# Optimization experiments

Measured on AMD Instinct MI355X. Metric: run time of the kernel, lower is better.

The kernel has to match this reference:

```python
import jax, jax.numpy as jnp
import numpy as np

D_MODEL = 512
HIDDEN = 2 * D_MODEL
B, L = 8, 2048
R_MIN, R_MAX = 0.8, 0.99
LN_EPS = 1e-5


def setup_inputs() -> dict:
    key = jax.random.key(0)
    ks = jax.random.split(key, 12)
    x = jax.random.normal(ks[0], (B, L, D_MODEL), jnp.float32)
    mask = jnp.ones((B, L), jnp.float32)
    # LRU eigenvalue init, exactly as the torch __init__
    u1 = jax.random.uniform(ks[1], (HIDDEN,), jnp.float32)
    u2 = jax.random.uniform(ks[2], (HIDDEN,), jnp.float32)
    nu_log = jnp.log(-0.5 * jnp.log(u1 * (R_MAX ** 2 - R_MIN ** 2) + R_MIN ** 2))
    theta_log = jnp.log(u2 * 2.0 * np.pi)
    diag_lambda = jnp.exp(jax.lax.complex(-jnp.exp(nu_log), jnp.exp(theta_log)))
    gamma_log = jnp.log(jnp.sqrt(1.0 - jnp.abs(diag_lambda) ** 2))
    params_log = jnp.stack([nu_log, theta_log, gamma_log])  # (3, HIDDEN)
    s_in = 1.0 / np.sqrt(D_MODEL)
    s_out = 1.0 / np.sqrt(HIDDEN)
    # complex Linear weights (real+imag parts; trained weights are fully complex)
    W_in_re = jax.random.uniform(ks[3], (HIDDEN, D_MODEL), jnp.float32, -s_in, s_in)
    W_in_im = jax.random.uniform(ks[4], (HIDDEN, D_MODEL), jnp.float32, -s_in, s_in)
    b_in_re = jax.random.uniform(ks[5], (HIDDEN,), jnp.float32, -s_in, s_in)
    b_in_im = jax.random.uniform(ks[6], (HIDDEN,), jnp.float32, -s_in, s_in)
    W_out_re = jax.random.uniform(ks[7], (D_MODEL, HIDDEN), jnp.float32, -s_out, s_out)
    W_out_im = jax.random.uniform(ks[8], (D_MODEL, HIDDEN), jnp.float32, -s_out, s_out)
    b_out_re = jax.random.uniform(ks[9], (D_MODEL,), jnp.float32, -s_out, s_out)
    b_out_im = jax.random.uniform(ks[10], (D_MODEL,), jnp.float32, -s_out, s_out)
    ln_w = jnp.ones((D_MODEL,), jnp.float32)
    ln_b = jnp.zeros((D_MODEL,), jnp.float32)
    return dict(x=x, mask=mask, params_log=params_log,
                W_in_re=W_in_re, W_in_im=W_in_im, b_in_re=b_in_re, b_in_im=b_in_im,
                W_out_re=W_out_re, W_out_im=W_out_im, b_out_re=b_out_re, b_out_im=b_out_im,
                ln_w=ln_w, ln_b=ln_b)


def _lru_parallel_scan(h, lamb, mask, Bn, Ln, Dn):
    # log-depth doubling trick over complex diagonal recurrence (faithful port)
    log2_L = int(np.ceil(np.log2(Ln)))
    for i in range(1, log2_L + 1):
        l = 2 ** i
        h = h.reshape(Bn * Ln // l, l, Dn)
        m = mask.reshape(Bn * Ln // l, l)
        h1, h2 = h[:, : l // 2], h[:, l // 2 :]
        if i > 1:
            lamb = jnp.concatenate([lamb, lamb * lamb[-1]], axis=0)  # powers lam^1..lam^(l/2)
        h2 = h2 + lamb * h1[:, -1:] * m[:, l // 2 - 1 : l // 2, None]
        h = jnp.concatenate([h1, h2], axis=1)
    return h.reshape(Bn, Ln, Dn)


def reference(x, mask, params_log, W_in_re, W_in_im, b_in_re, b_in_im,
              W_out_re, W_out_im, b_out_re, b_out_im, ln_w, ln_b):
    nu, theta, gamma = jnp.exp(params_log)  # each (HIDDEN,)
    lamb = jnp.exp(jax.lax.complex(-nu, theta))[None, :]  # (1, HIDDEN)
    W_in = jax.lax.complex(W_in_re, W_in_im)
    b_in = jax.lax.complex(b_in_re, b_in_im)
    W_out = jax.lax.complex(W_out_re, W_out_im)
    b_out = jax.lax.complex(b_out_re, b_out_im)
    xc = x.astype(jnp.complex64)
    h = (jnp.einsum('bld,hd->blh', xc, W_in) + b_in) * gamma  # (B, L, HIDDEN) complex64
    Bn, Ln, Dn = h.shape
    h = _lru_parallel_scan(h, lamb, mask, Bn, Ln, Dn)
    y = (jnp.einsum('blh,dh->bld', h, W_out) + b_out).real + x  # dropout = identity (eval)
    mean = jnp.mean(y, axis=-1, keepdims=True)
    var = jnp.var(y, axis=-1, keepdims=True)
    return (y - mean) / jnp.sqrt(var + LN_EPS) * ln_w + ln_b
```

## Files before the change

kernel.cpp:

```cpp
#include <hip/hip_runtime.h>
#include <hip/hip_bf16.h>
#include <cstdint>
#include <cstddef>


typedef unsigned short u16;
typedef __attribute__((ext_vector_type(8))) short bf16x8;
typedef __attribute__((ext_vector_type(4))) float f32x4;

#define B_    8
#define L_    2048
#define D_    512
#define H_    1024
#define M_    (B_ * L_)
#define SEG_  64
#define T_    (L_ / SEG_)

__device__ __forceinline__ float b2f(u16 u) {
  union { unsigned int i; float f; } v; v.i = ((unsigned int)u) << 16; return v.f;
}
__device__ __forceinline__ u16 f2b(float f) {
  union { float f; unsigned int i; } v; v.f = f;
  unsigned int x = v.i;
  return (u16)((x + 0x7fffu + ((x >> 16) & 1u)) >> 16);
}

__device__ __forceinline__ void gl2lds16(const void* g, void* l) {
  __builtin_amdgcn_global_load_lds(
      (const __attribute__((address_space(1))) void*)g,
      (__attribute__((address_space(3))) void*)l, 16, 0, 0);
}

__device__ __forceinline__ int ksw8(int row, int c) {
  return (c ^ (row & 7)) & 7;
}

__global__ __launch_bounds__(256) void prep_all(
    const float* __restrict__ x, u16* __restrict__ xb,
    const float* __restrict__ wire, const float* __restrict__ wiim,
    const float* __restrict__ wore, const float* __restrict__ woim,
    const float* __restrict__ bire, const float* __restrict__ biim,
    const float* __restrict__ params,
    u16* __restrict__ winb, u16* __restrict__ wcat, float* __restrict__ bb)
{
  int i = blockIdx.x * 256 + threadIdx.x;
#pragma unroll
  for (int j = 0; j < 4; ++j) {
    int gi = i + j * 524288;
    float4 v = ((const float4*)x)[gi];
    ushort4 o;
    o.x = f2b(v.x); o.y = f2b(v.y); o.z = f2b(v.z); o.w = f2b(v.w);
    ((ushort4*)xb)[gi] = o;
  }
  {
    int cp = i >> 9, k = i & 511;
    float g = expf(params[2 * H_ + cp]);
    winb[(size_t)(2 * cp) * 512 + k]     = f2b(wire[i] * g);
    winb[(size_t)(2 * cp + 1) * 512 + k] = f2b(wiim[i] * g);
  }
  {
    int d = i >> 10, c = i & 1023;
    wcat[(size_t)d * 2048 + 2 * c]     = f2b(wore[i]);
    wcat[(size_t)d * 2048 + 2 * c + 1] = f2b(-woim[i]);
  }
  if (i < 1024) {
    float gb = expf(params[2 * H_ + i]);
    bb[2 * i]     = bire[i] * gb;
    bb[2 * i + 1] = biim[i] * gb;
  }
}

__global__ __launch_bounds__(256, 4) void gemm_scan(
    const u16* __restrict__ A, const u16* __restrict__ Bp,
    const float* __restrict__ mask, const float* __restrict__ params,
    u16* __restrict__ h, const float* __restrict__ bb,
    float2* __restrict__ segfin, float* __restrict__ prodm)
{
  __shared__ __align__(16) u16 sAB[16384];
  __shared__ float mf[128];
  const int K = 512;

  const int tid  = threadIdx.x;
  const int lane = tid & 63;
  const int wave = tid >> 6;
  const int wm = wave >> 1, wn = wave & 1;
  const int m0 = blockIdx.x * 128;
  const int n0 = blockIdx.y * 128;
  const int b  = m0 >> 11;
  const int local0 = m0 & (L_ - 1);

  f32x4 acc[4][4];
#pragma unroll
  for (int i = 0; i < 4; ++i)
#pragma unroll
    for (int j = 0; j < 4; ++j) { f32x4 z = {0.f, 0.f, 0.f, 0.f}; acc[i][j] = z; }

  const int q = lane >> 4;
  const int r = lane & 15;

  for (int k0 = 0; k0 < K; k0 += 64) {
#pragma unroll
    for (int it = 0; it < 4; ++it) {
      int ci  = it * 256 + tid;
      int row = ci >> 3;
      int kc  = ksw8(row, ci & 7);
      gl2lds16(A  + (size_t)(m0 + row) * K + k0 + kc * 8, &sAB[ci * 8]);
      gl2lds16(Bp + (size_t)(n0 + row) * K + k0 + kc * 8, &sAB[8192 + ci * 8]);
    }
    __syncthreads();
#pragma unroll
    for (int kk = 0; kk < 2; ++kk) {
      const int cs = kk * 4 + q;
      bf16x8 af[4], bfv[4];
#pragma unroll
      for (int mt = 0; mt < 4; ++mt) {
        int arow = wm * 64 + mt * 16 + r;
        af[mt] = *(const bf16x8*)&sAB[(arow * 8 + ksw8(arow, cs)) * 8];
      }
#pragma unroll
      for (int nt = 0; nt < 4; ++nt) {
        int brow = wn * 64 + nt * 16 + r;
        bfv[nt] = *(const bf16x8*)&sAB[8192 + (brow * 8 + ksw8(brow, cs)) * 8];
      }
#pragma unroll
      for (int mt = 0; mt < 4; ++mt)
#pragma unroll
        for (int nt = 0; nt < 4; ++nt)
          acc[mt][nt] = __builtin_amdgcn_mfma_f32_16x16x32_bf16(
              bfv[nt], af[mt], acc[mt][nt], 0, 0, 0);
    }
    __syncthreads();
  }

  u16* sH = sAB;
  if (tid < 128)
    mf[tid] = (local0 + tid == 0) ? 0.f
                                  : mask[b * L_ + local0 + tid - 1];
#pragma unroll
  for (int mt = 0; mt < 4; ++mt) {
    const int trow = wm * 64 + mt * 16 + r;
    const int sw = (trow & 7) << 4;
#pragma unroll
    for (int nt = 0; nt < 4; ++nt) {
      const int nc = wn * 64 + nt * 16 + q * 4;
      const float4 b4 = *(const float4*)&bb[n0 + nc];
      ushort4 o;
      o.x = f2b(acc[mt][nt][0] + b4.x);
      o.y = f2b(acc[mt][nt][1] + b4.y);
      o.z = f2b(acc[mt][nt][2] + b4.z);
      o.w = f2b(acc[mt][nt][3] + b4.w);
      *(ushort4*)&sH[trow * 128 + (nc ^ sw)] = o;
    }
  }
  __syncthreads();

#pragma unroll
  for (int it = 0; it < 8; ++it) {
    int flat = it * 256 + tid;
    int row  = flat >> 4;
    int c16  = (flat & 15) * 8;
    bf16x8 v = *(const bf16x8*)&sH[row * 128 + (c16 ^ ((row & 7) << 4))];
    *(bf16x8*)&h[(size_t)(m0 + row) * 2048 + n0 + c16] = v;
  }

  {
    const int sIdx = wave;
    const int cpG  = (n0 >> 1) + lane;
    float nu = expf(params[cpG]);
    float th = expf(params[H_ + cpG]);
    float mg = expf(-nu);
    float lr = mg * cosf(th), li = mg * sinf(th);
    float sr = 0.f, si = 0.f, pm = 1.f;
    const int rbase = sIdx * 32;
#pragma unroll
    for (int t = 0; t < 32; ++t) {
      int row = rbase + t;
      int pos = row * 128 + ((lane * 2) ^ ((row & 7) << 4));
      ushort2 v = *(const ushort2*)&sH[pos];
      float fac = mf[row];
      pm *= fac;
      float nr = b2f(v.x) + fac * (lr * sr - li * si);
      float ni = b2f(v.y) + fac * (lr * si + li * sr);
      sr = nr; si = ni;
    }
    const int sG = (local0 >> 5) + sIdx;
    segfin[(size_t)(b * SEG_ + sG) * H_ + cpG] = make_float2(sr, si);
    if (lane == 0 && n0 == 0) prodm[b * SEG_ + sG] = pm;
  }
}

__global__ __launch_bounds__(256) void scan_carry(
    const float2* __restrict__ segfin, const float* __restrict__ prodm,
    const float* __restrict__ params, float2* __restrict__ carries)
{
  int idx = blockIdx.x * 256 + threadIdx.x;
  int b = idx >> 10, cp = idx & 1023;
  float nu = expf(params[cp]);
  float th = expf(params[H_ + cp]);
  float mg = expf(-nu);
  float ltr = mg * cosf(th), lti = mg * sinf(th);
#pragma unroll
  for (int sq = 0; sq < 5; ++sq) {
    float nr = ltr * ltr - lti * lti;
    float ni = 2.f * ltr * lti;
    ltr = nr; lti = ni;
  }
  float cr = 0.f, ci = 0.f;
  float2 fin = segfin[(size_t)(b * SEG_) * H_ + cp];
  float pmv = prodm[b * SEG_];
  for (int s = 0; s < SEG_; ++s) {
    size_t o = (size_t)(b * SEG_ + s) * H_ + cp;
    carries[o] = make_float2(cr, ci);
    float2 finn; float pmn;
    if (s + 1 < SEG_) { finn = segfin[o + H_]; pmn = prodm[b * SEG_ + s + 1]; }
    float nr = fin.x + pmv * (ltr * cr - lti * ci);
    float ni = fin.y + pmv * (ltr * ci + lti * cr);
    cr = nr; ci = ni;
    fin = finn; pmv = pmn;
  }
}

__global__ __launch_bounds__(256) void scan_full(
    u16* __restrict__ h, const float* __restrict__ mask,
    const float* __restrict__ params, const float2* __restrict__ carries)
{
  const int s = blockIdx.x, b = blockIdx.y;
  const int pa = threadIdx.x * 4;
  float lr[4], li[4], sr[4], si[4];
#pragma unroll
  for (int j = 0; j < 4; ++j) {
    int cp = pa + j;
    float nu = expf(params[cp]);
    float th = expf(params[H_ + cp]);
    float mg = expf(-nu);
    lr[j] = mg * cosf(th);
    li[j] = mg * sinf(th);
    float2 cv = carries[(size_t)(b * SEG_ + s) * H_ + cp];
    sr[j] = cv.x; si[j] = cv.y;
  }
  const int t0 = s * T_;
  u16* p = h + (size_t)(b * L_ + t0) * 2048 + pa * 2;
  const float* mp = mask + b * L_ + t0;
  float fac0;
  if (t0 == 0) fac0 = 0.f; else fac0 = mask[b * L_ + t0 - 1];

  bf16x8 buf[2][8];
#pragma unroll
  for (int j = 0; j < 8; ++j)
    buf[0][j] = *(const bf16x8*)(p + (size_t)j * 2048);
#pragma unroll
  for (int ch = 0; ch < T_ / 8; ++ch) {
    const int cur = ch & 1, nxt = cur ^ 1;
    if (ch < T_ / 8 - 1) {
      u16* pn = p + (size_t)(ch + 1) * 8 * 2048;
#pragma unroll
      for (int j = 0; j < 8; ++j)
        buf[nxt][j] = *(const bf16x8*)(pn + (size_t)j * 2048);
    }
#pragma unroll
    for (int j = 0; j < 8; ++j) {
      int i = ch * 8 + j;
      float fac = (i == 0) ? fac0 : mp[i - 1];
      u16 vv[8], ov[8];
      *(bf16x8*)vv = buf[cur][j];
#pragma unroll
      for (int k = 0; k < 4; ++k) {
        float ar = fac * sr[k], ai = fac * si[k];
        float nr = b2f(vv[2 * k])     + lr[k] * ar - li[k] * ai;
        float ni = b2f(vv[2 * k + 1]) + lr[k] * ai + li[k] * ar;
        sr[k] = nr; si[k] = ni;
        ov[2 * k]     = f2b(nr);
        ov[2 * k + 1] = f2b(ni);
      }
      *(bf16x8*)(p + (size_t)i * 2048) = *(bf16x8*)ov;
    }
  }
}

__global__ __launch_bounds__(256, 4) void gemm2(
    const u16* __restrict__ A, const u16* __restrict__ Bp, int K,
    float* __restrict__ outp, int ldc, const float* __restrict__ p0)
{
  __shared__ __align__(16) u16 sA[128 * 64];
  __shared__ __align__(16) u16 sB[128 * 64];

  const int tid  = threadIdx.x;
  const int lane = tid & 63;
  const int wave = tid >> 6;
  const int wm = wave >> 1, wn = wave & 1;
  const int m0 = blockIdx.x * 128;
  const int n0 = blockIdx.y * 128;

  f32x4 acc[4][4];
#pragma unroll
  for (int i = 0; i < 4; ++i)
#pragma unroll
    for (int j = 0; j < 4; ++j) { f32x4 z = {0.f, 0.f, 0.f, 0.f}; acc[i][j] = z; }

  const int q = lane >> 4;
  const int r = lane & 15;

  for (int k0 = 0; k0 < K; k0 += 64) {
#pragma unroll
    for (int it = 0; it < 4; ++it) {
      int ci  = it * 256 + tid;
      int row = ci >> 3;
      int kc  = ksw8(row, ci & 7);
      gl2lds16(A  + (size_t)(m0 + row) * K + k0 + kc * 8, &sA[ci * 8]);
      gl2lds16(Bp + (size_t)(n0 + row) * K + k0 + kc * 8, &sB[ci * 8]);
    }
    __syncthreads();
#pragma unroll
    for (int kk = 0; kk < 2; ++kk) {
      const int cs = kk * 4 + q;
      bf16x8 af[4], bfv[4];
#pragma unroll
      for (int mt = 0; mt < 4; ++mt) {
        int arow = wm * 64 + mt * 16 + r;
        af[mt] = *(const bf16x8*)&sA[(arow * 8 + ksw8(arow, cs)) * 8];
      }
#pragma unroll
      for (int nt = 0; nt < 4; ++nt) {
        int brow = wn * 64 + nt * 16 + r;
        bfv[nt] = *(const bf16x8*)&sB[(brow * 8 + ksw8(brow, cs)) * 8];
      }
#pragma unroll
      for (int mt = 0; mt < 4; ++mt)
#pragma unroll
        for (int nt = 0; nt < 4; ++nt)
          acc[mt][nt] = __builtin_amdgcn_mfma_f32_16x16x32_bf16(
              bfv[nt], af[mt], acc[mt][nt], 0, 0, 0);
    }
    __syncthreads();
  }

#pragma unroll
  for (int nt = 0; nt < 4; ++nt) {
    const int nb4 = n0 + wn * 64 + nt * 16 + q * 4;
    const float4 b4 = *(const float4*)&p0[nb4];
#pragma unroll
    for (int mt = 0; mt < 4; ++mt) {
      const int mg = m0 + wm * 64 + mt * 16 + r;
      float4 o;
      o.x = acc[mt][nt][0] + b4.x;
      o.y = acc[mt][nt][1] + b4.y;
      o.z = acc[mt][nt][2] + b4.z;
      o.w = acc[mt][nt][3] + b4.w;
      *(float4*)&outp[(size_t)mg * ldc + nb4] = o;
    }
  }
}

__global__ __launch_bounds__(256) void ln_kernel(
    const float* __restrict__ y, const float* __restrict__ xg,
    const float* __restrict__ lnw, const float* __restrict__ lnb,
    float* __restrict__ out)
{
  const int wave = threadIdx.x >> 6, lane = threadIdx.x & 63;
  const size_t row = (size_t)blockIdx.x * 4 + wave;
  const float* yr = y + row * 512;
  const float* xr = xg + row * 512;
  float z[8];
  { float4 t = *(const float4*)&yr[lane * 4];        z[0]=t.x; z[1]=t.y; z[2]=t.z; z[3]=t.w; }
  { float4 t = *(const float4*)&yr[256 + lane * 4];  z[4]=t.x; z[5]=t.y; z[6]=t.z; z[7]=t.w; }
  { float4 t = *(const float4*)&xr[lane * 4];        z[0]+=t.x; z[1]+=t.y; z[2]+=t.z; z[3]+=t.w; }
  { float4 t = *(const float4*)&xr[256 + lane * 4];  z[4]+=t.x; z[5]+=t.y; z[6]+=t.z; z[7]+=t.w; }
  float s = 0.f, ss = 0.f;
#pragma unroll
  for (int j = 0; j < 8; ++j) { s += z[j]; ss += z[j] * z[j]; }
#pragma unroll
  for (int o = 32; o > 0; o >>= 1) { s += __shfl_xor(s, o); ss += __shfl_xor(ss, o); }
  const float mean = s * (1.f / 512.f);
  const float var  = ss * (1.f / 512.f) - mean * mean;
  const float inv  = rsqrtf(var + 1e-5f);
  float ov[8];
#pragma unroll
  for (int j = 0; j < 8; ++j) {
    int col = (j < 4) ? (lane * 4 + j) : (256 + lane * 4 + (j - 4));
    ov[j] = (z[j] - mean) * inv * lnw[col] + lnb[col];
  }
  { float4 t; t.x=ov[0]; t.y=ov[1]; t.z=ov[2]; t.w=ov[3];
    *(float4*)&out[row * 512 + lane * 4] = t; }
  { float4 t; t.x=ov[4]; t.y=ov[5]; t.z=ov[6]; t.w=ov[7];
    *(float4*)&out[row * 512 + 256 + lane * 4] = t; }
}

extern "C" void kernel_launch(void* const* d_in, const int* in_sizes, int n_in,
                              void* d_out, int out_size, void* d_ws, size_t ws_size,
                              hipStream_t stream) {
  (void)in_sizes; (void)n_in; (void)out_size; (void)ws_size;
  const float* x      = (const float*)d_in[0];
  const float* mask   = (const float*)d_in[1];
  const float* params = (const float*)d_in[2];
  const float* Wire   = (const float*)d_in[3];
  const float* Wiim   = (const float*)d_in[4];
  const float* bire   = (const float*)d_in[5];
  const float* biim   = (const float*)d_in[6];
  const float* Wore   = (const float*)d_in[7];
  const float* Woim   = (const float*)d_in[8];
  const float* bore   = (const float*)d_in[9];
  const float* lnw    = (const float*)d_in[11];
  const float* lnb    = (const float*)d_in[12];

  char* ws = (char*)d_ws;
  u16*    xb      = (u16*)   (ws);
  float*  y       = (float*) (ws);
  float2* segfin  = (float2*)(ws + (size_t)16777216);
  float2* carries = (float2*)(ws + (size_t)20971520);
  float*  prodm   = (float*) (ws + (size_t)25165824);
  u16*    h       = (u16*)   (ws + (size_t)33554432);
  u16*    winb    = (u16*)   (ws + (size_t)100663296);
  u16*    wcat    = (u16*)   (ws + (size_t)102760448);
  float*  bb      = (float*) (ws + (size_t)104857600);

  prep_all<<<2048, 256, 0, stream>>>(x, xb, Wire, Wiim, Wore, Woim,
                                     bire, biim, params, winb, wcat, bb);

  gemm_scan<<<dim3(128, 16), 256, 0, stream>>>(
      xb, winb, mask, params, h, bb, segfin, prodm);

  scan_carry<<<32, 256, 0, stream>>>(segfin, prodm, params, carries);
  scan_full<<<dim3(SEG_, B_), 256, 0, stream>>>(h, mask, params, carries);

  gemm2<<<dim3(128, 4), 256, 0, stream>>>(h, wcat, 2048, y, 512, bore);

  ln_kernel<<<4096, 256, 0, stream>>>(y, x, lnw, lnb, (float*)d_out);
}
```

Before: 240.0 us.

## Raise GEMM occupancy, broadcast mask via shuffles, and widen scan kernel parallelism

The mask shared-memory array in gemm_scan is replaced by a per-lane register load that is broadcast with __shfl, which trims LDS use, and both GEMMs raise their launch-bounds occupancy hint from 4 to 5. scan_carry moves to 64-thread blocks so its 32 blocks become 128, and scan_full splits the channels into two halves per batch so each thread handles 2 complex pairs instead of 4. The aim is more concurrent work on the latency-bound scan kernels and better GEMM occupancy. The trade-off is possible register pressure or spills under the tighter bounds, and narrower 8-byte memory accesses in scan_full.

```diff
diff --git a/kernel.cpp b/kernel.cpp
--- a/kernel.cpp
+++ b/kernel.cpp
@@ -70,14 +70,13 @@
   }
 }
 
-__global__ __launch_bounds__(256, 4) void gemm_scan(
+__global__ __launch_bounds__(256, 5) void gemm_scan(
     const u16* __restrict__ A, const u16* __restrict__ Bp,
     const float* __restrict__ mask, const float* __restrict__ params,
     u16* __restrict__ h, const float* __restrict__ bb,
     float2* __restrict__ segfin, float* __restrict__ prodm)
 {
   __shared__ __align__(16) u16 sAB[16384];
-  __shared__ float mf[128];
   const int K = 512;
 
   const int tid  = threadIdx.x;
@@ -133,9 +132,6 @@
   }
 
   u16* sH = sAB;
-  if (tid < 128)
-    mf[tid] = (local0 + tid == 0) ? 0.f
-                                  : mask[b * L_ + local0 + tid - 1];
 #pragma unroll
   for (int mt = 0; mt < 4; ++mt) {
     const int trow = wm * 64 + mt * 16 + r;
@@ -166,18 +162,23 @@
   {
     const int sIdx = wave;
     const int cpG  = (n0 >> 1) + lane;
+    const int rbase = sIdx * 32;
+    float mv = 0.f;
+    if (lane < 32) {
+      int g = local0 + rbase + lane;
+      mv = (g == 0) ? 0.f : mask[b * L_ + g - 1];
+    }
     float nu = expf(params[cpG]);
     float th = expf(params[H_ + cpG]);
     float mg = expf(-nu);
     float lr = mg * cosf(th), li = mg * sinf(th);
     float sr = 0.f, si = 0.f, pm = 1.f;
-    const int rbase = sIdx * 32;
 #pragma unroll
     for (int t = 0; t < 32; ++t) {
       int row = rbase + t;
       int pos = row * 128 + ((lane * 2) ^ ((row & 7) << 4));
       ushort2 v = *(const ushort2*)&sH[pos];
-      float fac = mf[row];
+      float fac = __shfl(mv, t);
       pm *= fac;
       float nr = b2f(v.x) + fac * (lr * sr - li * si);
       float ni = b2f(v.y) + fac * (lr * si + li * sr);
@@ -189,11 +190,11 @@
   }
 }
 
-__global__ __launch_bounds__(256) void scan_carry(
+__global__ __launch_bounds__(64) void scan_carry(
     const float2* __restrict__ segfin, const float* __restrict__ prodm,
     const float* __restrict__ params, float2* __restrict__ carries)
 {
-  int idx = blockIdx.x * 256 + threadIdx.x;
+  int idx = blockIdx.x * 64 + threadIdx.x;
   int b = idx >> 10, cp = idx & 1023;
   float nu = expf(params[cp]);
   float th = expf(params[H_ + cp]);
@@ -224,11 +225,13 @@
     u16* __restrict__ h, const float* __restrict__ mask,
     const float* __restrict__ params, const float2* __restrict__ carries)
 {
-  const int s = blockIdx.x, b = blockIdx.y;
-  const int pa = threadIdx.x * 4;
-  float lr[4], li[4], sr[4], si[4];
-#pragma unroll
-  for (int j = 0; j < 4; ++j) {
+  const int s = blockIdx.x;
+  const int bh = blockIdx.y;
+  const int b = bh >> 1, half = bh & 1;
+  const int pa = half * 512 + threadIdx.x * 2;
+  float lr[2], li[2], sr[2], si[2];
+#pragma unroll
+  for (int j = 0; j < 2; ++j) {
     int cp = pa + j;
     float nu = expf(params[cp]);
     float th = expf(params[H_ + cp]);
@@ -244,10 +247,10 @@
   float fac0;
   if (t0 == 0) fac0 = 0.f; else fac0 = mask[b * L_ + t0 - 1];
 
-  bf16x8 buf[2][8];
+  ushort4 buf[2][8];
 #pragma unroll
   for (int j = 0; j < 8; ++j)
-    buf[0][j] = *(const bf16x8*)(p + (size_t)j * 2048);
+    buf[0][j] = *(const ushort4*)(p + (size_t)j * 2048);
 #pragma unroll
   for (int ch = 0; ch < T_ / 8; ++ch) {
     const int cur = ch & 1, nxt = cur ^ 1;
@@ -255,16 +258,16 @@
       u16* pn = p + (size_t)(ch + 1) * 8 * 2048;
 #pragma unroll
       for (int j = 0; j < 8; ++j)
-        buf[nxt][j] = *(const bf16x8*)(pn + (size_t)j * 2048);
+        buf[nxt][j] = *(const ushort4*)(pn + (size_t)j * 2048);
     }
 #pragma unroll
     for (int j = 0; j < 8; ++j) {
       int i = ch * 8 + j;
       float fac = (i == 0) ? fac0 : mp[i - 1];
-      u16 vv[8], ov[8];
-      *(bf16x8*)vv = buf[cur][j];
-#pragma unroll
-      for (int k = 0; k < 4; ++k) {
+      u16 vv[4], ov[4];
+      *(ushort4*)vv = buf[cur][j];
+#pragma unroll
+      for (int k = 0; k < 2; ++k) {
         float ar = fac * sr[k], ai = fac * si[k];
         float nr = b2f(vv[2 * k])     + lr[k] * ar - li[k] * ai;
         float ni = b2f(vv[2 * k + 1]) + lr[k] * ai + li[k] * ar;
@@ -272,17 +275,16 @@
         ov[2 * k]     = f2b(nr);
         ov[2 * k + 1] = f2b(ni);
       }
-      *(bf16x8*)(p + (size_t)i * 2048) = *(bf16x8*)ov;
-    }
-  }
-}
-
-__global__ __launch_bounds__(256, 4) void gemm2(
+      *(ushort4*)(p + (size_t)i * 2048) = *(ushort4*)ov;
+    }
+  }
+}
+
+__global__ __launch_bounds__(256, 5) void gemm2(
     const u16* __restrict__ A, const u16* __restrict__ Bp, int K,
     float* __restrict__ outp, int ldc, const float* __restrict__ p0)
 {
-  __shared__ __align__(16) u16 sA[128 * 64];
-  __shared__ __align__(16) u16 sB[128 * 64];
+  __shared__ __align__(16) u16 sAB[16384];
 
   const int tid  = threadIdx.x;
   const int lane = tid & 63;
@@ -306,8 +308,8 @@
       int ci  = it * 256 + tid;
       int row = ci >> 3;
       int kc  = ksw8(row, ci & 7);
-      gl2lds16(A  + (size_t)(m0 + row) * K + k0 + kc * 8, &sA[ci * 8]);
-      gl2lds16(Bp + (size_t)(n0 + row) * K + k0 + kc * 8, &sB[ci * 8]);
+      gl2lds16(A  + (size_t)(m0 + row) * K + k0 + kc * 8, &sAB[ci * 8]);
+      gl2lds16(Bp + (size_t)(n0 + row) * K + k0 + kc * 8, &sAB[8192 + ci * 8]);
     }
     __syncthreads();
 #pragma unroll
@@ -317,12 +319,12 @@
 #pragma unroll
       for (int mt = 0; mt < 4; ++mt) {
         int arow = wm * 64 + mt * 16 + r;
-        af[mt] = *(const bf16x8*)&sA[(arow * 8 + ksw8(arow, cs)) * 8];
+        af[mt] = *(const bf16x8*)&sAB[(arow * 8 + ksw8(arow, cs)) * 8];
       }
 #pragma unroll
       for (int nt = 0; nt < 4; ++nt) {
         int brow = wn * 64 + nt * 16 + r;
-        bfv[nt] = *(const bf16x8*)&sB[(brow * 8 + ksw8(brow, cs)) * 8];
+        bfv[nt] = *(const bf16x8*)&sAB[8192 + (brow * 8 + ksw8(brow, cs)) * 8];
       }
 #pragma unroll
       for (int mt = 0; mt < 4; ++mt)
@@ -419,8 +421,8 @@
   gemm_scan<<<dim3(128, 16), 256, 0, stream>>>(
       xb, winb, mask, params, h, bb, segfin, prodm);
 
-  scan_carry<<<32, 256, 0, stream>>>(segfin, prodm, params, carries);
-  scan_full<<<dim3(SEG_, B_), 256, 0, stream>>>(h, mask, params, carries);
+  scan_carry<<<128, 64, 0, stream>>>(segfin, prodm, params, carries);
+  scan_full<<<dim3(SEG_, B_ * 2), 256, 0, stream>>>(h, mask, params, carries);
 
   gemm2<<<dim3(128, 4), 256, 0, stream>>>(h, wcat, 2048, y, 512, bore);
 
```

Result: slower. 421.2 us (+75.5%).
